# Optimization experiments

Measured on AMD Instinct MI355X. Metric: run time of the kernel, lower is better.

## Reference

```python
import jax, jax.numpy as jnp
import numpy as np

MOMENTUM = 0.99
EPS = 1e-5


def setup_inputs() -> dict:
    key = jax.random.key(0)
    k1, k2, k3, k4 = jax.random.split(key, 4)
    x = jax.random.normal(k1, (16, 256, 64, 64), dtype=jnp.float32)
    embed = jax.random.normal(k2, (2048, 256), dtype=jnp.float32)
    cluster_size = jax.random.uniform(k3, (2048,), dtype=jnp.float32)
    embed_avg = jax.random.normal(k4, (256, 2048), dtype=jnp.float32)
    return {"x": x, "embed": embed, "cluster_size": cluster_size, "embed_avg": embed_avg}


def reference(x, embed, cluster_size, embed_avg):
    # x: (b, c, h, w) with c == emb_dim; embed: (D, c)
    b, c, h, w = x.shape
    D = embed.shape[0]
    # flatten exactly as the torch code: transpose(1,-1) then reshape(-1, c)
    flat = jnp.swapaxes(x, 1, 3).reshape(-1, c)  # (N, c), N = b*w*h
    # L2 kNN with k=1, expressed as argmax of 2*q.k - |k|^2 - |q|^2 (as in _torch_knn)
    scores = (2.0 * (flat @ embed.T)
              - jnp.sum(embed * embed, axis=1)[None, :]
              - jnp.sum(flat * flat, axis=1, keepdims=True))  # (N, D)
    ids_flat = jnp.argmax(scores, axis=1)  # (N,)
    ids = ids_flat.reshape(b, h, w)
    # lookup + transpose(1,-1), mirroring the original op sequence
    quantized = jnp.swapaxes(embed[ids], 1, 3)  # (b, c, w, h) == (b, c, h, w) since h == w
    commit_loss = jnp.mean((x - quantized) ** 2)
    # EMA statistics (training branch). one-hot matmul expressed as segment sums (same math).
    onehot_sum = jax.ops.segment_sum(jnp.ones_like(ids_flat, dtype=flat.dtype), ids_flat,
                                     num_segments=D)  # (D,)
    embed_sum = jax.ops.segment_sum(flat, ids_flat, num_segments=D).T  # (c, D) == flat.T @ onehot
    new_cluster_size = MOMENTUM * cluster_size + (1.0 - MOMENTUM) * onehot_sum
    new_embed_avg = MOMENTUM * embed_avg + (1.0 - MOMENTUM) * embed_sum
    n = jnp.sum(new_cluster_size)
    cs_smoothed = n * (new_cluster_size + EPS) / (n + D * EPS)
    new_embed = new_embed_avg.T / cs_smoothed[:, None]  # (D, c)
    return quantized, commit_loss, ids, new_embed, new_cluster_size, new_embed_avg
```

## Files before the change

### kernel.cpp

```cpp
#include <hip/hip_runtime.h>

#define D_CODES 2048
#define C_DIM   256
#define MOM     0.99f
#define ONE_M   0.01f
#define EPSI    1e-5f
#define TAU     0.16f
#define RCAP    16384
#define SBCAP   2304

#define Q_OFF    0
#define LOSS_OFF 16777216
#define IDS_OFF  16777217
#define NE_OFF   16842753
#define NCS_OFF  17367041
#define NEA_OFF  17369089

#define WS_ICNT    0
#define WS_CNTF    2048
#define WS_OFFS    4096
#define WS_CURS    6144
#define WS_SUMX2   10240
#define WS_NTOT    11264
#define WS_RCNT    11268
#define WS_NSB     11269
#define WS_NORMS   11272
#define WS_RLIST   13320
#define WS_ESUM    29704
#define WS_E2      553992
#define WS_KEYH    816136
#define WS_M2H     1340424
#define WS_PLIST   1602568
#define WS_SBCODE  1668104
#define WS_SBSTART 1670408
#define WS_SBINFO  1672712
#define WS_LOSSP   1675016

typedef _Float16 half8 __attribute__((ext_vector_type(8)));
typedef __attribute__((ext_vector_type(4))) float f32x4;
typedef unsigned long long u64;

__device__ __forceinline__ f32x4 MFH(half8 a, half8 b, f32x4 c) {
    return __builtin_amdgcn_mfma_f32_16x16x32_f16(a, b, c, 0, 0, 0);
}
__device__ __forceinline__ unsigned enc_f(float v) {
    unsigned u = __float_as_uint(v);
    return (u & 0x80000000u) ? ~u : (u | 0x80000000u);
}
__device__ __forceinline__ float dec_f(unsigned u) {
    return (u & 0x80000000u) ? __uint_as_float(u & 0x7FFFFFFFu)
                             : __uint_as_float(~u);
}
__device__ __forceinline__ unsigned short h_bits(_Float16 h) {
    union { _Float16 f; unsigned short u; } c; c.f = h; return c.u;
}

__global__ __launch_bounds__(256) void k_init(
    const float* __restrict__ embed, const float* __restrict__ x,
    float* __restrict__ e2f, float* __restrict__ norms,
    float* __restrict__ esum, int* __restrict__ icnt,
    float* __restrict__ lossp, unsigned* __restrict__ rcnt,
    float* __restrict__ etg, unsigned short* __restrict__ xt2,
    float* __restrict__ sumx2p)
{
    __shared__ float sh[8228];
    const int b = blockIdx.x, t = threadIdx.x;
    esum[(size_t)b * 256 + t] = 0.f;
    if (b < 64) {
        if (t < 32) sh[t] = 0.f;
        __syncthreads();
        char* e2 = (char*)e2f;
        const int s = b;
        #pragma unroll
        for (int it = 0; it < 4; ++it) {
            int u = it * 256 + t;
            int r = u >> 9, kc = (u >> 6) & 7, l = u & 63;
            int code = s * 32 + r * 16 + (l & 15);
            int ch0  = kc * 32 + ((l >> 4) << 3);
            const float* src = embed + (size_t)code * C_DIM + ch0;
            float4 v0 = *(const float4*)src;
            float4 v1 = *(const float4*)(src + 4);
            float vv[8] = {v0.x, v0.y, v0.z, v0.w, v1.x, v1.y, v1.z, v1.w};
            half8 hh;
            float p = 0.f;
            #pragma unroll
            for (int j = 0; j < 8; ++j) { hh[j] = (_Float16)vv[j]; p += vv[j] * vv[j]; }
            atomicAdd(&sh[r * 16 + (l & 15)], p);
            char* dst = e2 + (size_t)s * 16384 + (size_t)((r * 8 + kc) * 64 + l) * 16;
            *(half8*)dst = hh;
        }
        __syncthreads();
        if (t < 32) norms[s * 32 + t] = sh[t];
    } else if (b < 72) {
        icnt[(b - 64) * 256 + t] = 0;
    } else if (b < 81) {
        int j = (b - 72) * 256 + t;
        if (j < SBCAP) lossp[j] = 0.f;
    } else if (b == 81) {
        if (t == 0) *rcnt = 0u;
    } else if (b >= 128 && b < 384) {
        int code0 = (b - 128) * 8;
        #pragma unroll
        for (int j = 0; j < 8; ++j) {
            float v = embed[(size_t)(code0 + j) * C_DIM + t];
            etg[(size_t)t * D_CODES + code0 + j] = v;
        }
    } else if (b >= 384 && b < 1408) {
        float (*xs2)[257] = (float(*)[257])sh;
        float* wred = sh + 8224;
        const int xb = b - 384;
        const int bi = xb >> 6;
        const int hi = xb & 63;
        const int wl = t & 31;
        const int chh = t >> 5;
        float sx2 = 0.f;
        #pragma unroll
        for (int pass = 0; pass < 2; ++pass) {
            __syncthreads();
            #pragma unroll 8
            for (int k = 0; k < 32; ++k) {
                int ch = k * 8 + chh;
                float v = x[((size_t)(bi * C_DIM + ch)) * 4096 + hi * 64 + pass * 32 + wl];
                sx2 += v * v;
                xs2[wl][ch] = v;
            }
            __syncthreads();
            const int pxl = t >> 7;
            const int ch2 = (t & 127) * 2;
            #pragma unroll 4
            for (int j2 = 0; j2 < 16; ++j2) {
                int pl = j2 * 2 + pxl;
                float v0 = xs2[pl][ch2];
                float v1 = xs2[pl][ch2 + 1];
                unsigned pack = ((unsigned)h_bits((_Float16)v1) << 16)
                              | h_bits((_Float16)v0);
                size_t n = (size_t)bi * 4096 + (size_t)(pass * 32 + pl) * 64 + hi;
                *(unsigned*)(xt2 + n * C_DIM + ch2) = pack;
            }
        }
        #pragma unroll
        for (int o = 32; o; o >>= 1) sx2 += __shfl_down(sx2, o);
        __syncthreads();
        if ((t & 63) == 0) wred[t >> 6] = sx2;
        __syncthreads();
        if (t == 0) sumx2p[xb] = wred[0] + wred[1] + wred[2] + wred[3];
    }
}

__global__ __launch_bounds__(256, 1) void k_main(
    const unsigned short* __restrict__ xt2, const float* __restrict__ e2f,
    const float* __restrict__ norms, u64* __restrict__ keyh,
    float* __restrict__ m2h)
{
    __shared__ float nlds[512];
    const int t  = threadIdx.x;
    const int l  = t & 63;
    const int w  = __builtin_amdgcn_readfirstlane(t >> 6);
    const int blk = blockIdx.x;
    const int p  = blk & 3;
    const int q  = (blk >> 2) & 15;
    const int bi = blk >> 6;
    const char* e2 = (const char*)e2f + (size_t)p * 262144 + (size_t)l * 16;

    if (t < 128) *(float4*)&nlds[t * 4] = *(const float4*)(norms + p * 512 + t * 4);

    half8 bx[4][8];
    {
        const _Float16* xth = (const _Float16*)xt2;
        #pragma unroll
        for (int nt = 0; nt < 4; ++nt) {
            int wi = nt * 16 + (l & 15);
            size_t n = (size_t)bi * 4096 + (size_t)wi * 64 + 4 * q + w;
            const _Float16* base = xth + n * C_DIM + ((l >> 4) << 3);
            #pragma unroll
            for (int c = 0; c < 8; ++c)
                bx[nt][c] = *(const half8*)(base + c * 32);
        }
    }
    __syncthreads();

    float m1[4] = {-3.4e38f, -3.4e38f, -3.4e38f, -3.4e38f};
    float m2[4] = {-3.4e38f, -3.4e38f, -3.4e38f, -3.4e38f};
    int   i1[4] = {0, 0, 0, 0};

    half8 ahA[8], ahB[8];
    auto loadbuf = [&](half8* buf, int ri) {
        const char* pp = e2 + (size_t)ri * 8192;
        #pragma unroll
        for (int kc = 0; kc < 8; ++kc)
            buf[kc] = *(const half8*)(pp + kc * 1024);
    };
    auto compute = [&](const half8* ah, int ri) {
        float4 nrm = *(const float4*)&nlds[ri * 16 + ((l >> 4) << 2)];
        f32x4 z = {0.f, 0.f, 0.f, 0.f};
        f32x4 aA[4] = {z, z, z, z};
        #pragma unroll
        for (int kc = 0; kc < 8; ++kc) {
            #pragma unroll
            for (int nt = 0; nt < 4; ++nt)
                aA[nt] = MFH(ah[kc], bx[nt][kc], aA[nt]);
        }
        int c0 = p * 512 + ri * 16 + ((l >> 4) << 2);
        float nr[4] = {nrm.x, nrm.y, nrm.z, nrm.w};
        #pragma unroll
        for (int nt = 0; nt < 4; ++nt) {
            #pragma unroll
            for (int reg = 0; reg < 4; ++reg) {
                float sc = 2.f * aA[nt][reg] - nr[reg];
                int code = c0 + reg;
                if (sc > m1[nt]) { m2[nt] = m1[nt]; m1[nt] = sc; i1[nt] = code; }
                else             { m2[nt] = fmaxf(m2[nt], sc); }
            }
        }
    };

    loadbuf(ahA, 0);
    for (int ri = 0; ri < 32; ri += 2) {
        loadbuf(ahB, ri + 1);
        compute(ahA, ri);
        if (ri + 2 < 32) loadbuf(ahA, ri + 2);
        compute(ahB, ri + 1);
    }

    #pragma unroll
    for (int nt = 0; nt < 4; ++nt) {
        float a1 = m1[nt], a2 = m2[nt];
        int   ai = i1[nt];
        #pragma unroll
        for (int off = 16; off <= 32; off <<= 1) {
            float o1 = __shfl_xor(a1, off);
            int   oi = __shfl_xor(ai, off);
            float o2 = __shfl_xor(a2, off);
            if (o1 > a1)       { a2 = fmaxf(a1, o2); a1 = o1; ai = oi; }
            else if (o1 == a1) { if (oi < ai) ai = oi; a2 = a1; }
            else               { a2 = fmaxf(a2, o1); }
        }
        if (l < 16) {
            int wi = nt * 16 + l;
            int hi_ = 4 * q + w;
            int n = (bi << 12) + (wi << 6) + hi_;
            keyh[((size_t)p << 16) + n] = ((u64)enc_f(a1) << 32) | (unsigned)(~ai);
            m2h[(p << 16) + n] = a2;
        }
    }
}

__global__ __launch_bounds__(256) void k_merge(
    const u64* __restrict__ keyh, const float* __restrict__ m2h,
    float* __restrict__ out, int* __restrict__ icnt,
    unsigned* __restrict__ rcnt, int* __restrict__ rlist)
{
    int n = blockIdx.x * 256 + threadIdx.x;
    u64 k0 = keyh[n],          k1 = keyh[65536 + n];
    u64 k2 = keyh[131072 + n], k3 = keyh[196608 + n];
    float q0 = m2h[n],          q1 = m2h[65536 + n];
    float q2 = m2h[131072 + n], q3 = m2h[196608 + n];
    bool a01 = k0 >= k1;
    u64  kp01 = a01 ? k0 : k1;
    float sec01 = fmaxf(a01 ? q0 : q1, dec_f((unsigned)((a01 ? k1 : k0) >> 32)));
    bool a23 = k2 >= k3;
    u64  kp23 = a23 ? k2 : k3;
    float sec23 = fmaxf(a23 ? q2 : q3, dec_f((unsigned)((a23 ? k3 : k2) >> 32)));
    bool aW = kp01 >= kp23;
    u64  kW = aW ? kp01 : kp23;
    float second = fmaxf(aW ? sec01 : sec23,
                         dec_f((unsigned)((aW ? kp23 : kp01) >> 32)));
    float sW = dec_f((unsigned)(kW >> 32));
    int code = (int)(~(unsigned)kW);
    out[IDS_OFF + n] = (float)code;
    atomicAdd(&icnt[code], 1);
    if (sW - second < TAU) {
        unsigned j = atomicAdd(rcnt, 1u);
        if (j < RCAP) rlist[j] = n;
    }
}

__global__ __launch_bounds__(256) void k_rescue(
    const float* __restrict__ x, const float* __restrict__ etg,
    const float* __restrict__ norms, const unsigned* __restrict__ rcnt,
    const int* __restrict__ rlist, float* __restrict__ out,
    int* __restrict__ icnt)
{
    __shared__ float xs[8][257];
    __shared__ int nn[8];
    __shared__ u64 rk[4][8];
    const int t = threadIdx.x;
    const int l = t & 63;
    const int w = t >> 6;
    int nf = (int)min(*rcnt, (unsigned)RCAP);
    int nch = (nf + 7) >> 3;
    for (int chunk = blockIdx.x; chunk < nch; chunk += gridDim.x) {
        __syncthreads();
        if (t < 8) {
            int idx = chunk * 8 + t;
            nn[t] = rlist[idx < nf ? idx : (nf - 1)];
        }
        __syncthreads();
        #pragma unroll
        for (int p = 0; p < 8; ++p) {
            int n = nn[p];
            int bi = n >> 12, wi = (n >> 6) & 63, hi = n & 63;
            xs[p][t] = x[((size_t)(bi * C_DIM + t)) * 4096 + hi * 64 + wi];
        }
        __syncthreads();
        u64 bk[8];
        #pragma unroll
        for (int p = 0; p < 8; ++p) bk[p] = 0ull;
        #pragma unroll
        for (int rep = 0; rep < 2; ++rep) {
            const int d0 = rep * 1024 + t * 4;
            f32x4 acc[8];
            #pragma unroll
            for (int p = 0; p < 8; ++p) acc[p] = (f32x4){0.f, 0.f, 0.f, 0.f};
            for (int c = 0; c < C_DIM; ++c) {
                float4 e4 = *(const float4*)(etg + (size_t)c * D_CODES + d0);
                f32x4 ev = {e4.x, e4.y, e4.z, e4.w};
                #pragma unroll
                for (int p = 0; p < 8; ++p)
                    acc[p] += xs[p][c] * ev;
            }
            float4 nr = *(const float4*)(norms + d0);
            float nrr[4] = {nr.x, nr.y, nr.z, nr.w};
            #pragma unroll
            for (int p = 0; p < 8; ++p) {
                #pragma unroll
                for (int j = 0; j < 4; ++j) {
                    float sc = 2.f * acc[p][j] - nrr[j];
                    u64 key = ((u64)enc_f(sc) << 32) | (unsigned)(~(d0 + j));
                    if (key > bk[p]) bk[p] = key;
                }
            }
        }
        #pragma unroll
        for (int p = 0; p < 8; ++p) {
            u64 k0 = bk[p];
            #pragma unroll
            for (int o = 32; o; o >>= 1) {
                u64 ok = __shfl_down(k0, o);
                if (ok > k0) k0 = ok;
            }
            if (l == 0) rk[w][p] = k0;
        }
        __syncthreads();
        if (t < 8 && chunk * 8 + t < nf) {
            u64 k0 = rk[0][t];
            if (rk[1][t] > k0) k0 = rk[1][t];
            if (rk[2][t] > k0) k0 = rk[2][t];
            if (rk[3][t] > k0) k0 = rk[3][t];
            int n = nn[t];
            int newid = (int)(~(unsigned)k0);
            int old = (int)out[IDS_OFF + n];
            if (newid != old) {
                out[IDS_OFF + n] = (float)newid;
                atomicAdd(&icnt[old], -1);
                atomicAdd(&icnt[newid], 1);
            }
        }
    }
}

__global__ __launch_bounds__(256) void k_prefix(const int* __restrict__ icnt,
                                                const float* __restrict__ cs_in,
                                                int* __restrict__ offs,
                                                int* __restrict__ curs,
                                                float* __restrict__ cntf,
                                                int* __restrict__ sbcode,
                                                int* __restrict__ sbstart,
                                                int* __restrict__ sbinfo,
                                                int* __restrict__ nsbtot,
                                                float* __restrict__ ntot) {
    __shared__ int ps[256];
    __shared__ float fs[256];
    const int t = threadIdx.x;
    int c[8], o8[8];
    int s = 0;
    #pragma unroll
    for (int j = 0; j < 8; ++j) c[j] = icnt[t * 8 + j];
    #pragma unroll
    for (int j = 0; j < 8; ++j) { int tmp = c[j]; c[j] = s; s += tmp; }
    ps[t] = s;
    __syncthreads();
    for (int off = 1; off < 256; off <<= 1) {
        int v = (t >= off) ? ps[t - off] : 0;
        __syncthreads();
        ps[t] += v;
        __syncthreads();
    }
    int base = ps[t] - s;
    #pragma unroll
    for (int j = 0; j < 8; ++j) {
        int o = base + c[j];
        o8[j] = o;
        offs[t * 8 + j] = o;
        curs[t * 8 + j] = o;
        cntf[t * 8 + j] = (float)(icnt[t * 8 + j]);
    }
    int s2 = 0;
    int nb[8];
    #pragma unroll
    for (int j = 0; j < 8; ++j) {
        int cnt = icnt[t * 8 + j];
        nb[j] = (cnt + 255) >> 8;
        s2 += nb[j];
    }
    __syncthreads();
    ps[t] = s2;
    __syncthreads();
    for (int off = 1; off < 256; off <<= 1) {
        int v = (t >= off) ? ps[t - off] : 0;
        __syncthreads();
        ps[t] += v;
        __syncthreads();
    }
    int pos = ps[t] - s2;
    #pragma unroll
    for (int j = 0; j < 8; ++j) {
        int code = t * 8 + j;
        int cnt = icnt[code];
        int n = nb[j];
        for (int k = 0; k < n; ++k) {
            sbcode[pos]  = code;
            sbstart[pos] = o8[j] + k * 256;
            int len = cnt - k * 256; if (len > 256) len = 256;
            sbinfo[pos]  = len | ((n > 1) ? (1 << 16) : 0);
            ++pos;
        }
    }
    if (t == 255) *nsbtot = ps[255];
    float s3 = 0.f;
    #pragma unroll
    for (int j = 0; j < 8; ++j) s3 += cs_in[t * 8 + j];
    fs[t] = s3;
    __syncthreads();
    for (int o = 128; o; o >>= 1) { if (t < o) fs[t] += fs[t + o]; __syncthreads(); }
    if (t == 0) *ntot = MOM * fs[0] + ONE_M * 65536.0f;
}

__global__ __launch_bounds__(256) void k_scatter(const float* __restrict__ out,
                                                 int* __restrict__ curs,
                                                 int* __restrict__ plist) {
    int n = blockIdx.x * 256 + threadIdx.x;
    int id = (int)out[IDS_OFF + n];
    int pos = atomicAdd(&curs[id], 1);
    plist[pos] = n;
}

__global__ __launch_bounds__(256) void k_esum(
    const unsigned short* __restrict__ xt2, const float* __restrict__ embed,
    const float* __restrict__ norms, const int* __restrict__ sbcode,
    const int* __restrict__ sbstart, const int* __restrict__ sbinfo,
    const int* __restrict__ plist, const int* __restrict__ nsbtot,
    float* __restrict__ esum, float* __restrict__ lossp)
{
    __shared__ int   ns[256];
    __shared__ float red[256];
    const _Float16* xth = (const _Float16*)xt2;
    const int t = threadIdx.x;
    const int total = *nsbtot;
    for (int sb = blockIdx.x; sb < total; sb += gridDim.x) {
        const int d     = sbcode[sb];
        const int start = sbstart[sb];
        const int info  = sbinfo[sb];
        const int len   = info & 0xFFFF;
        const bool multi = (info >> 16) != 0;
        __syncthreads();
        if (t < len) ns[t] = plist[start + t];
        __syncthreads();
        float acc = 0.f;
        #pragma unroll 8
        for (int i = 0; i < len; ++i)
            acc += (float)xth[(size_t)ns[i] * C_DIM + t];
        if (multi) atomicAdd(&esum[(size_t)t * D_CODES + d], acc);
        else       esum[(size_t)t * D_CODES + d] = acc;
        red[t] = acc * embed[(size_t)d * C_DIM + t];
        __syncthreads();
        for (int o = 128; o; o >>= 1) {
            if (t < o) red[t] += red[t + o];
            __syncthreads();
        }
        if (t == 0) lossp[sb] = 2.f * red[0] - (float)len * norms[d];
    }
}

__global__ __launch_bounds__(256) void k_post(
    const float* __restrict__ embed, const float* __restrict__ cs_in,
    const float* __restrict__ cntf, const float* __restrict__ embed_avg,
    const float* __restrict__ esum, const float* __restrict__ ntotp,
    const float* __restrict__ lossp, const float* __restrict__ sumx2p,
    float* __restrict__ out)
{
    __shared__ float shm[8456];
    const int b = blockIdx.x;
    const int t = threadIdx.x;
    if (b < 1024) {
        int* ids_s = (int*)shm;
        float (*es)[257] = (float(*)[257])(shm + 64);
        const int bi = b >> 6;
        const int hi = b & 63;
        const int wl = t & 31;
        const int cg = t >> 5;
        if (t < 64) ids_s[t] = (int)out[IDS_OFF + ((size_t)bi << 12) + (t << 6) + hi];
        __syncthreads();
        #pragma unroll
        for (int pass = 0; pass < 2; ++pass) {
            #pragma unroll 8
            for (int p = 0; p < 32; ++p) {
                es[p][t] = embed[(size_t)ids_s[pass * 32 + p] * C_DIM + t];
            }
            __syncthreads();
            #pragma unroll 8
            for (int k = 0; k < 32; ++k) {
                int ch = k * 8 + cg;
                out[Q_OFF + ((size_t)(bi * C_DIM + ch)) * 4096 + hi * 64 + pass * 32 + wl]
                    = es[wl][ch];
            }
            __syncthreads();
        }
    } else if (b < 3072) {
        int bb = b - 1024;
        int ch = bb >> 3;
        int d  = ((bb & 7) << 8) + t;
        float ntot = *ntotp;
        float ncs  = MOM * cs_in[d] + ONE_M * cntf[d];
        if (bb < 8) out[NCS_OFF + d] = ncs;
        float csm  = ntot * (ncs + EPSI) / (ntot + (float)D_CODES * EPSI);
        size_t i = (size_t)ch * D_CODES + d;
        float nea = MOM * embed_avg[i] + ONE_M * esum[i];
        out[NEA_OFF + i] = nea;
        out[NE_OFF + (size_t)d * C_DIM + ch] = nea / csm;
    } else {
        float* sm = shm;
        float s1 = 0.f;
        for (int i = t; i < 1024; i += 256) s1 += sumx2p[i];
        float s2 = 0.f;
        for (int i = t; i < SBCAP; i += 256) s2 += lossp[i];
        sm[t] = s1 - s2;
        __syncthreads();
        for (int o = 128; o; o >>= 1) { if (t < o) sm[t] += sm[t + o]; __syncthreads(); }
        if (t == 0) out[LOSS_OFF] = sm[0] / 16777216.f;
    }
}

extern "C" void kernel_launch(void* const* d_in, const int* in_sizes, int n_in,
                              void* d_out, int out_size, void* d_ws, size_t ws_size,
                              hipStream_t stream) {
    const float* x     = (const float*)d_in[0];
    const float* embed = (const float*)d_in[1];
    const float* cs    = (const float*)d_in[2];
    const float* ea    = (const float*)d_in[3];
    float* out = (float*)d_out;
    float* ws  = (float*)d_ws;
    int*      icnt    = (int*)(ws + WS_ICNT);
    float*    cntf    = ws + WS_CNTF;
    int*      offs    = (int*)(ws + WS_OFFS);
    int*      curs    = (int*)(ws + WS_CURS);
    float*    sumx2p  = ws + WS_SUMX2;
    float*    ntot    = ws + WS_NTOT;
    unsigned* rcnt    = (unsigned*)(ws + WS_RCNT);
    int*      nsbtot  = (int*)(ws + WS_NSB);
    float*    norms   = ws + WS_NORMS;
    int*      rlist   = (int*)(ws + WS_RLIST);
    float*    esum    = ws + WS_ESUM;
    float*    e2      = ws + WS_E2;
    u64*      keyh    = (u64*)(ws + WS_KEYH);
    float*    m2h     = ws + WS_M2H;
    int*      plist   = (int*)(ws + WS_PLIST);
    int*      sbcode  = (int*)(ws + WS_SBCODE);
    int*      sbstart = (int*)(ws + WS_SBSTART);
    int*      sbinfo  = (int*)(ws + WS_SBINFO);
    float*    lossp   = ws + WS_LOSSP;
    unsigned short* xt2 = (unsigned short*)(out + Q_OFF);
    float*    etg     = out + NEA_OFF;

    k_init<<<2048, 256, 0, stream>>>(embed, x, e2, norms, esum, icnt, lossp, rcnt,
                                     etg, xt2, sumx2p);
    k_main<<<1024, 256, 0, stream>>>(xt2, e2, norms, keyh, m2h);
    k_merge<<<256, 256, 0, stream>>>(keyh, m2h, out, icnt, rcnt, rlist);
    k_rescue<<<512, 256, 0, stream>>>(x, etg, norms, rcnt, rlist, out, icnt);
    k_prefix<<<1, 256, 0, stream>>>(icnt, cs, offs, curs, cntf, sbcode, sbstart,
                                    sbinfo, nsbtot, ntot);
    k_scatter<<<256, 256, 0, stream>>>(out, curs, plist);
    k_esum<<<SBCAP, 256, 0, stream>>>(xt2, embed, norms, sbcode, sbstart, sbinfo,
                                      plist, nsbtot, esum, lossp);
    k_post<<<3073, 256, 0, stream>>>(embed, cs, cntf, ea, esum, ntot, lossp,
                                     sumx2p, out);
}
```

Before: 278.0 us.

## Double per-wave query tile in k_main and use LDS histogram in k_merge

Each wave in the main distance kernel now holds 8 query tiles instead of 4, so every codebook fragment loaded from memory feeds twice as many MFMA ops. The grid is halved to match, which cuts total codebook traffic. The cost is many more registers (bx and accumulators double), which may cause spills or lower occupancy. Separately, k_merge builds a per-block shared-memory histogram of codes and flushes the non-zero bins to global memory, replacing one global atomic per point.

```diff
diff --git a/kernel.cpp b/kernel.cpp
--- a/kernel.cpp
+++ b/kernel.cpp
@@ -158,19 +158,20 @@
     const int w  = __builtin_amdgcn_readfirstlane(t >> 6);
     const int blk = blockIdx.x;
     const int p  = blk & 3;
-    const int q  = (blk >> 2) & 15;
-    const int bi = blk >> 6;
+    const int q  = (blk >> 2) & 7;
+    const int bi = blk >> 5;
     const char* e2 = (const char*)e2f + (size_t)p * 262144 + (size_t)l * 16;
 
     if (t < 128) *(float4*)&nlds[t * 4] = *(const float4*)(norms + p * 512 + t * 4);
 
-    half8 bx[4][8];
+    half8 bx[8][8];
     {
         const _Float16* xth = (const _Float16*)xt2;
         #pragma unroll
-        for (int nt = 0; nt < 4; ++nt) {
-            int wi = nt * 16 + (l & 15);
-            size_t n = (size_t)bi * 4096 + (size_t)wi * 64 + 4 * q + w;
+        for (int nt = 0; nt < 8; ++nt) {
+            int wi = (nt & 3) * 16 + (l & 15);
+            int hi = 8 * q + 2 * w + (nt >> 2);
+            size_t n = (size_t)bi * 4096 + (size_t)wi * 64 + hi;
             const _Float16* base = xth + n * C_DIM + ((l >> 4) << 3);
             #pragma unroll
             for (int c = 0; c < 8; ++c)
@@ -179,9 +180,10 @@
     }
     __syncthreads();
 
-    float m1[4] = {-3.4e38f, -3.4e38f, -3.4e38f, -3.4e38f};
-    float m2[4] = {-3.4e38f, -3.4e38f, -3.4e38f, -3.4e38f};
-    int   i1[4] = {0, 0, 0, 0};
+    float m1[8], m2[8];
+    int   i1[8];
+    #pragma unroll
+    for (int nt = 0; nt < 8; ++nt) { m1[nt] = -3.4e38f; m2[nt] = -3.4e38f; i1[nt] = 0; }
 
     half8 ahA[8], ahB[8];
     auto loadbuf = [&](half8* buf, int ri) {
@@ -193,17 +195,17 @@
     auto compute = [&](const half8* ah, int ri) {
         float4 nrm = *(const float4*)&nlds[ri * 16 + ((l >> 4) << 2)];
         f32x4 z = {0.f, 0.f, 0.f, 0.f};
-        f32x4 aA[4] = {z, z, z, z};
+        f32x4 aA[8] = {z, z, z, z, z, z, z, z};
         #pragma unroll
         for (int kc = 0; kc < 8; ++kc) {
             #pragma unroll
-            for (int nt = 0; nt < 4; ++nt)
+            for (int nt = 0; nt < 8; ++nt)
                 aA[nt] = MFH(ah[kc], bx[nt][kc], aA[nt]);
         }
         int c0 = p * 512 + ri * 16 + ((l >> 4) << 2);
         float nr[4] = {nrm.x, nrm.y, nrm.z, nrm.w};
         #pragma unroll
-        for (int nt = 0; nt < 4; ++nt) {
+        for (int nt = 0; nt < 8; ++nt) {
             #pragma unroll
             for (int reg = 0; reg < 4; ++reg) {
                 float sc = 2.f * aA[nt][reg] - nr[reg];
@@ -223,7 +225,7 @@
     }
 
     #pragma unroll
-    for (int nt = 0; nt < 4; ++nt) {
+    for (int nt = 0; nt < 8; ++nt) {
         float a1 = m1[nt], a2 = m2[nt];
         int   ai = i1[nt];
         #pragma unroll
@@ -236,9 +238,9 @@
             else               { a2 = fmaxf(a2, o1); }
         }
         if (l < 16) {
-            int wi = nt * 16 + l;
-            int hi_ = 4 * q + w;
-            int n = (bi << 12) + (wi << 6) + hi_;
+            int wi = (nt & 3) * 16 + l;
+            int hi = 8 * q + 2 * w + (nt >> 2);
+            int n = (bi << 12) + (wi << 6) + hi;
             keyh[((size_t)p << 16) + n] = ((u64)enc_f(a1) << 32) | (unsigned)(~ai);
             m2h[(p << 16) + n] = a2;
         }
@@ -250,7 +252,12 @@
     float* __restrict__ out, int* __restrict__ icnt,
     unsigned* __restrict__ rcnt, int* __restrict__ rlist)
 {
-    int n = blockIdx.x * 256 + threadIdx.x;
+    __shared__ int hist[D_CODES];
+    const int t = threadIdx.x;
+    #pragma unroll
+    for (int j = 0; j < 8; ++j) hist[j * 256 + t] = 0;
+    __syncthreads();
+    int n = blockIdx.x * 256 + t;
     u64 k0 = keyh[n],          k1 = keyh[65536 + n];
     u64 k2 = keyh[131072 + n], k3 = keyh[196608 + n];
     float q0 = m2h[n],          q1 = m2h[65536 + n];
@@ -268,10 +275,16 @@
     float sW = dec_f((unsigned)(kW >> 32));
     int code = (int)(~(unsigned)kW);
     out[IDS_OFF + n] = (float)code;
-    atomicAdd(&icnt[code], 1);
+    atomicAdd(&hist[code], 1);
     if (sW - second < TAU) {
         unsigned j = atomicAdd(rcnt, 1u);
         if (j < RCAP) rlist[j] = n;
+    }
+    __syncthreads();
+    #pragma unroll
+    for (int j = 0; j < 8; ++j) {
+        int c = hist[j * 256 + t];
+        if (c) atomicAdd(&icnt[j * 256 + t], c);
     }
 }
 
@@ -574,7 +587,7 @@
 
     k_init<<<2048, 256, 0, stream>>>(embed, x, e2, norms, esum, icnt, lossp, rcnt,
                                      etg, xt2, sumx2p);
-    k_main<<<1024, 256, 0, stream>>>(xt2, e2, norms, keyh, m2h);
+    k_main<<<512, 256, 0, stream>>>(xt2, e2, norms, keyh, m2h);
     k_merge<<<256, 256, 0, stream>>>(keyh, m2h, out, icnt, rcnt, rlist);
     k_rescue<<<512, 256, 0, stream>>>(x, etg, norms, rcnt, rlist, out, icnt);
     k_prefix<<<1, 256, 0, stream>>>(icnt, cs, offs, curs, cntf, sbcode, sbstart,
```

Measured after the change: 285.4 us. +2.6%, slower.
